# Optimization experiments

Hardware: AMD Instinct MI355X
Metric: run time of the kernel (lower is better)

Reference implementation:

```python
import jax, jax.numpy as jnp
import numpy as np

HIDDEN = 2048
HEADS = 16
HEAD_DIM = HIDDEN // HEADS  # 128
SCALE = 1.0 / float(np.sqrt(HEAD_DIM))
B, S = 2, 2048


def setup_inputs() -> dict:
    key = jax.random.key(0)
    ks = jax.random.split(key, 5)
    return {
        "x": jax.random.normal(ks[0], (B, S, HIDDEN), dtype=jnp.float32),
        "q_w": jax.random.normal(ks[1], (HIDDEN, HIDDEN), dtype=jnp.float32) * (HIDDEN ** -0.5),
        "k_w": jax.random.normal(ks[2], (HEAD_DIM, HIDDEN), dtype=jnp.float32) * (HIDDEN ** -0.5),
        "v_w": jax.random.normal(ks[3], (HEAD_DIM, HIDDEN), dtype=jnp.float32) * (HIDDEN ** -0.5),
        "o_w": jax.random.normal(ks[4], (HIDDEN, HIDDEN), dtype=jnp.float32) * (HIDDEN ** -0.5),
    }


def reference(x, q_w, k_w, v_w, o_w):
    b, s, _ = x.shape
    # torch F.linear: x @ W^T with W [out, in]
    q = (x @ q_w.T).reshape(b, s, HEADS, HEAD_DIM).transpose(0, 2, 1, 3)  # [B,H,S,D]
    k = x @ k_w.T  # [B,S,D] single shared KV head
    v = x @ v_w.T  # [B,S,D]
    # scores: [B,H,S,S] -- explicit O(S^2) materialization as in the source
    scores = jnp.einsum('bhqd,bkd->bhqk', q, k) * SCALE
    # softmax in float32 then cast back (matches dtype=torch.float32 then type_as)
    attn = jax.nn.softmax(scores.astype(jnp.float32), axis=-1).astype(q.dtype)
    out = jnp.einsum('bhqk,bkd->bhqd', attn, v)  # [B,H,S,D]
    out = out.transpose(0, 2, 1, 3).reshape(b, s, HIDDEN)
    return out @ o_w.T
```

## Files before the change

### kernel.cpp

```cpp
#include <hip/hip_runtime.h>
#include <stdint.h>

#define HID 2048
#define DHEAD 128
#define SEQL 2048
#define C2 0.1275187981510609f
#define MOFF 8.0f

typedef __attribute__((ext_vector_type(4))) float f32x4;
typedef __attribute__((ext_vector_type(8))) short s16x8;

__device__ __forceinline__ unsigned short bf16_rne(float f) {
  union { float f; unsigned u; } v; v.f = f;
  return (unsigned short)((v.u + 0x7FFFu + ((v.u >> 16) & 1u)) >> 16);
}

__device__ __forceinline__ void gload_lds16(const void* g, void* l) {
  __builtin_amdgcn_global_load_lds(
      (__attribute__((address_space(1))) unsigned int*)(void*)g,
      (__attribute__((address_space(3))) unsigned int*)l, 16, 0, 0);
}

__device__ __forceinline__ void cvt8(const float* __restrict__ in,
                                     unsigned short* __restrict__ out, int k) {
  const f32x4* p = (const f32x4*)in;
  f32x4 a = p[2 * k], b = p[2 * k + 1];
  union { s16x8 v; unsigned short s[8]; } o;
  o.s[0] = bf16_rne(a[0]); o.s[1] = bf16_rne(a[1]);
  o.s[2] = bf16_rne(a[2]); o.s[3] = bf16_rne(a[3]);
  o.s[4] = bf16_rne(b[0]); o.s[5] = bf16_rne(b[1]);
  o.s[6] = bf16_rne(b[2]); o.s[7] = bf16_rne(b[3]);
  ((s16x8*)out)[k] = o.v;
}

__global__ __launch_bounds__(256) void cvt_bf16_k(const float* __restrict__ in,
                                                  unsigned short* __restrict__ out,
                                                  int n8) {
  int i = blockIdx.x * 256 + threadIdx.x;
  if (i >= n8) return;
  cvt8(in, out, i);
}

__global__ __launch_bounds__(256) void cvt4_k(
    const float* __restrict__ s0, unsigned short* __restrict__ d0, int n0,
    const float* __restrict__ s1, unsigned short* __restrict__ d1, int n1,
    const float* __restrict__ s2, unsigned short* __restrict__ d2, int n2,
    const float* __restrict__ s3, unsigned short* __restrict__ d3, int n3) {
  int i = blockIdx.x * 256 + threadIdx.x;
  if (i < n0) { cvt8(s0, d0, i); return; }
  i -= n0;
  if (i < n1) { cvt8(s1, d1, i); return; }
  i -= n1;
  if (i < n2) { cvt8(s2, d2, i); return; }
  i -= n2;
  if (i < n3) { cvt8(s3, d3, i); return; }
}

template <int LOG2SLOTS>
__device__ __forceinline__ void stage_tile(const unsigned short* __restrict__ src,
                                           int ld, char* smem, int t) {
  int w = t >> 6;
#pragma unroll
  for (int i = 0; i < 4; ++i) {
    int c = i * 256 + t;
    int row = c >> LOG2SLOTS;
    int slot = c & ((1 << LOG2SLOTS) - 1);
    gload_lds16(src + row * ld + ((slot ^ (row & 7)) << 3),
                smem + (i * 256 + w * 64) * 16);
  }
}

template <int MODE>
__global__ __launch_bounds__(256, 2) void gemm_bt(
    const unsigned short* __restrict__ A, const unsigned short* __restrict__ Bw,
    void* __restrict__ Cout, int M, int N, int K,
    unsigned short* __restrict__ Kb, unsigned short* __restrict__ Vt) {
  __shared__ char As[2][16384];
  __shared__ char Bs[2][16384];
  int t = threadIdx.x;
  int lane = t & 63, w = t >> 6;
  int wm = w >> 1, wn = w & 1;
  int l15 = lane & 15, l4 = lane >> 4;

  int gdx = gridDim.x;
  int nwg = gdx * gridDim.y;
  int bid = blockIdx.y * gdx + blockIdx.x;
  int q8 = nwg >> 3;
  int swz = (bid & 7) * q8 + (bid >> 3);
  int tm = (swz / gdx) * 128, tn = (swz % gdx) * 128;

  f32x4 acc[4][4] = {};

  stage_tile<3>(A + tm * K, K, As[0], t);
  stage_tile<3>(Bw + tn * K, K, Bs[0], t);
  asm volatile("s_waitcnt vmcnt(0)" ::: "memory");
  __builtin_amdgcn_s_barrier();

  int nk = K >> 6;
  for (int ki = 0; ki < nk; ++ki) {
    int cur = ki & 1;
    if (ki + 1 < nk) {
      stage_tile<3>(A + tm * K + (ki + 1) * 64, K, As[cur ^ 1], t);
      stage_tile<3>(Bw + tn * K + (ki + 1) * 64, K, Bs[cur ^ 1], t);
    }
    const char* as = As[cur];
    const char* bs = Bs[cur];
    s16x8 af[4][2], bfr[4][2];
#pragma unroll
    for (int m = 0; m < 4; ++m)
#pragma unroll
      for (int kk = 0; kk < 2; ++kk) {
        int row = wm * 64 + m * 16 + l15;
        af[m][kk] = *(const s16x8*)(as + row * 128 + (((kk * 4 + l4) ^ (row & 7)) << 4));
      }
#pragma unroll
    for (int n = 0; n < 4; ++n)
#pragma unroll
      for (int kk = 0; kk < 2; ++kk) {
        int row = wn * 64 + n * 16 + l15;
        bfr[n][kk] = *(const s16x8*)(bs + row * 128 + (((kk * 4 + l4) ^ (row & 7)) << 4));
      }
    __builtin_amdgcn_s_setprio(1);
#pragma unroll
    for (int m = 0; m < 4; ++m)
#pragma unroll
      for (int n = 0; n < 4; ++n)
#pragma unroll
        for (int kk = 0; kk < 2; ++kk)
          acc[m][n] = __builtin_amdgcn_mfma_f32_16x16x32_bf16(af[m][kk], bfr[n][kk],
                                                              acc[m][n], 0, 0, 0);
    __builtin_amdgcn_s_setprio(0);
    asm volatile("s_waitcnt vmcnt(0) lgkmcnt(0)" ::: "memory");
    __builtin_amdgcn_sched_barrier(0);
    __builtin_amdgcn_s_barrier();
  }

#pragma unroll
  for (int m = 0; m < 4; ++m)
#pragma unroll
    for (int n = 0; n < 4; ++n) {
      int col = tn + wn * 64 + n * 16 + l15;
#pragma unroll
      for (int j = 0; j < 4; ++j) {
        int row = tm + wm * 64 + m * 16 + l4 * 4 + j;
        float v = acc[m][n][j];
        if (MODE == 1) {
          ((float*)Cout)[row * N + col] = v;
        } else {
          if (col < 2048) {
            ((unsigned short*)Cout)[row * 2048 + col] = bf16_rne(v);
          } else if (col < 2176) {
            Kb[row * 128 + (col - 2048)] = bf16_rne(v);
          } else {
            int d = col - 2176, bb = row >> 11, s = row & 2047;
            Vt[((bb * 128 + d) << 11) + s] = bf16_rne(v);
          }
        }
      }
    }
}

__global__ __launch_bounds__(256, 2) void attn_k(
    const unsigned short* __restrict__ Q, const unsigned short* __restrict__ Kb,
    const unsigned short* __restrict__ Vt, unsigned short* __restrict__ AO) {
  __shared__ char Ks[2][16384];
  __shared__ char Vs[2][16384];
  int t = threadIdx.x;
  int lane = t & 63, w = t >> 6;
  int l15 = lane & 15, l4 = lane >> 4;
  int qt = blockIdx.x, bh = blockIdx.y;
  int b = bh >> 4, h = bh & 15;
  int qg = b * SEQL + qt * 128 + w * 32;

  s16x8 qf[2][4];
#pragma unroll
  for (int m = 0; m < 2; ++m)
#pragma unroll
    for (int kc = 0; kc < 4; ++kc)
      qf[m][kc] = *(const s16x8*)(Q + (qg + m * 16 + l15) * HID + h * DHEAD + kc * 32 + l4 * 8);

  union { s16x8 v; unsigned short s[8]; } one_;
#pragma unroll
  for (int i = 0; i < 8; ++i) one_.s[i] = 0x3F80;
  const s16x8 ones = one_.v;

  f32x4 oacc[2][9] = {};

  {
#pragma unroll
    for (int i = 0; i < 4; ++i) {
      int c = i * 256 + t, row = c >> 4, slot = c & 15;
      gload_lds16(Kb + (b * SEQL + row) * DHEAD + ((slot ^ (row & 7)) << 3),
                  Ks[0] + (i * 256 + w * 64) * 16);
    }
#pragma unroll
    for (int i = 0; i < 4; ++i) {
      int c = i * 256 + t, row = c >> 3, slot = c & 7;
      gload_lds16(Vt + (b * DHEAD + row) * SEQL + ((slot ^ (row & 7)) << 3),
                  Vs[0] + (i * 256 + w * 64) * 16);
    }
  }
  asm volatile("s_waitcnt vmcnt(0)" ::: "memory");
  __builtin_amdgcn_s_barrier();

  for (int kv = 0; kv < SEQL; kv += 64) {
    int cur = (kv >> 6) & 1;
    if (kv + 64 < SEQL) {
#pragma unroll
      for (int i = 0; i < 4; ++i) {
        int c = i * 256 + t, row = c >> 4, slot = c & 15;
        gload_lds16(Kb + (b * SEQL + kv + 64 + row) * DHEAD + ((slot ^ (row & 7)) << 3),
                    Ks[cur ^ 1] + (i * 256 + w * 64) * 16);
      }
#pragma unroll
      for (int i = 0; i < 4; ++i) {
        int c = i * 256 + t, row = c >> 3, slot = c & 7;
        gload_lds16(Vt + (b * DHEAD + row) * SEQL + kv + 64 + ((slot ^ (row & 7)) << 3),
                    Vs[cur ^ 1] + (i * 256 + w * 64) * 16);
      }
    }

    const char* ks = Ks[cur];
    const char* vs = Vs[cur];
    char* Psw = Ks[cur] + w * 4096;

    f32x4 sacc[2][4] = {};
    __builtin_amdgcn_s_setprio(1);
#pragma unroll
    for (int n = 0; n < 4; ++n) {
      int krow = n * 16 + l15;
#pragma unroll
      for (int kc = 0; kc < 4; ++kc) {
        s16x8 kf = *(const s16x8*)(ks + krow * 256 + (((kc * 4 + l4) ^ (krow & 7)) << 4));
        sacc[0][n] = __builtin_amdgcn_mfma_f32_16x16x32_bf16(qf[0][kc], kf, sacc[0][n], 0, 0, 0);
        sacc[1][n] = __builtin_amdgcn_mfma_f32_16x16x32_bf16(qf[1][kc], kf, sacc[1][n], 0, 0, 0);
      }
    }
    __builtin_amdgcn_s_setprio(0);

    asm volatile("s_waitcnt lgkmcnt(0)" ::: "memory");
    __builtin_amdgcn_sched_barrier(0);
    __builtin_amdgcn_s_barrier();

#pragma unroll
    for (int m = 0; m < 2; ++m)
#pragma unroll
      for (int n = 0; n < 4; ++n) {
        int pcol = n * 16 + l15;
#pragma unroll
        for (int j = 0; j < 4; ++j) {
          float p = __builtin_amdgcn_exp2f(__builtin_fmaf(sacc[m][n][j], C2, -MOFF));
          int prow = m * 16 + l4 * 4 + j;
          *(unsigned short*)(Psw + prow * 128 + (((pcol >> 3) ^ (prow & 7)) << 4) +
                             (pcol & 7) * 2) = bf16_rne(p);
        }
      }

    asm volatile("s_waitcnt lgkmcnt(0)" ::: "memory");
    __builtin_amdgcn_sched_barrier(0);

#pragma unroll
    for (int kc2 = 0; kc2 < 2; ++kc2) {
      s16x8 pa[2];
#pragma unroll
      for (int m = 0; m < 2; ++m) {
        int row = m * 16 + l15;
        pa[m] = *(const s16x8*)(Psw + row * 128 + (((kc2 * 4 + l4) ^ (row & 7)) << 4));
      }
      __builtin_amdgcn_s_setprio(1);
#pragma unroll
      for (int n = 0; n < 8; ++n) {
        int vrow = n * 16 + l15;
        s16x8 vf = *(const s16x8*)(vs + vrow * 128 + (((kc2 * 4 + l4) ^ (vrow & 7)) << 4));
        oacc[0][n] = __builtin_amdgcn_mfma_f32_16x16x32_bf16(pa[0], vf, oacc[0][n], 0, 0, 0);
        oacc[1][n] = __builtin_amdgcn_mfma_f32_16x16x32_bf16(pa[1], vf, oacc[1][n], 0, 0, 0);
      }
      oacc[0][8] = __builtin_amdgcn_mfma_f32_16x16x32_bf16(pa[0], ones, oacc[0][8], 0, 0, 0);
      oacc[1][8] = __builtin_amdgcn_mfma_f32_16x16x32_bf16(pa[1], ones, oacc[1][8], 0, 0, 0);
      __builtin_amdgcn_s_setprio(0);
    }

    asm volatile("s_waitcnt vmcnt(0) lgkmcnt(0)" ::: "memory");
    __builtin_amdgcn_sched_barrier(0);
    __builtin_amdgcn_s_barrier();
  }

#pragma unroll
  for (int m = 0; m < 2; ++m) {
    float inv[4];
#pragma unroll
    for (int j = 0; j < 4; ++j) inv[j] = 1.f / oacc[m][8][j];
#pragma unroll
    for (int n = 0; n < 8; ++n) {
      int col = h * DHEAD + n * 16 + l15;
#pragma unroll
      for (int j = 0; j < 4; ++j) {
        int row = qg + m * 16 + l4 * 4 + j;
        AO[row * HID + col] = bf16_rne(oacc[m][n][j] * inv[j]);
      }
    }
  }
}

extern "C" void kernel_launch(void* const* d_in, const int* in_sizes, int n_in,
                              void* d_out, int out_size, void* d_ws, size_t ws_size,
                              hipStream_t stream) {
  const float* x  = (const float*)d_in[0];
  const float* qw = (const float*)d_in[1];
  const float* kw = (const float*)d_in[2];
  const float* vw = (const float*)d_in[3];
  const float* ow = (const float*)d_in[4];

  char* ws = (char*)d_ws;
  unsigned short* xb   = (unsigned short*)(ws);
  unsigned short* qwb  = (unsigned short*)(ws + 16777216);
  unsigned short* owb  = qwb;
  unsigned short* kvwb = (unsigned short*)(ws + 25165824);
  unsigned short* Qb   = (unsigned short*)(ws + 26214400);
  unsigned short* Kbuf = (unsigned short*)(ws + 42991616);
  unsigned short* Vtb  = (unsigned short*)(ws + 44040192);
  unsigned short* AOb  = xb;

  cvt4_k<<<6400, 256, 0, stream>>>(x, xb, 1048576, qw, qwb, 524288,
                                   kw, kvwb, 32768, vw, kvwb + 262144, 32768);

  gemm_bt<0><<<dim3(18, 32), 256, 0, stream>>>(xb, qwb, Qb, 4096, 2304, 2048, Kbuf, Vtb);
  cvt_bf16_k<<<2048, 256, 0, stream>>>(ow, owb, 524288);
  attn_k<<<dim3(16, 32), 256, 0, stream>>>(Qb, Kbuf, Vtb, AOb);
  gemm_bt<1><<<dim3(16, 32), 256, 0, stream>>>(AOb, owb, d_out, 4096, 2048, 2048,
                                               nullptr, nullptr);
}
```

Measured before the change: 215.6 us.

## Deepen GEMM prefetch pipeline and give attention P its own LDS buffer

```diff
diff --git a/kernel.cpp b/kernel.cpp
--- a/kernel.cpp
+++ b/kernel.cpp
@@ -9,6 +9,7 @@
 
 typedef __attribute__((ext_vector_type(4))) float f32x4;
 typedef __attribute__((ext_vector_type(8))) short s16x8;
+typedef __attribute__((ext_vector_type(2))) unsigned int u32x2;
 
 __device__ __forceinline__ unsigned short bf16_rne(float f) {
   union { float f; unsigned u; } v; v.f = f;
@@ -93,16 +94,17 @@
 
   stage_tile<3>(A + tm * K, K, As[0], t);
   stage_tile<3>(Bw + tn * K, K, Bs[0], t);
-  asm volatile("s_waitcnt vmcnt(0)" ::: "memory");
-  __builtin_amdgcn_s_barrier();
+  stage_tile<3>(A + tm * K + 64, K, As[1], t);
+  stage_tile<3>(Bw + tn * K + 64, K, Bs[1], t);
 
   int nk = K >> 6;
   for (int ki = 0; ki < nk; ++ki) {
     int cur = ki & 1;
-    if (ki + 1 < nk) {
-      stage_tile<3>(A + tm * K + (ki + 1) * 64, K, As[cur ^ 1], t);
-      stage_tile<3>(Bw + tn * K + (ki + 1) * 64, K, Bs[cur ^ 1], t);
-    }
+    if (ki < nk - 1) asm volatile("s_waitcnt vmcnt(8)" ::: "memory");
+    else             asm volatile("s_waitcnt vmcnt(0)" ::: "memory");
+    __builtin_amdgcn_sched_barrier(0);
+    __builtin_amdgcn_s_barrier();
+
     const char* as = As[cur];
     const char* bs = Bs[cur];
     s16x8 af[4][2], bfr[4][2];
@@ -120,6 +122,13 @@
         int row = wn * 64 + n * 16 + l15;
         bfr[n][kk] = *(const s16x8*)(bs + row * 128 + (((kk * 4 + l4) ^ (row & 7)) << 4));
       }
+    asm volatile("s_waitcnt lgkmcnt(0)" ::: "memory");
+    __builtin_amdgcn_sched_barrier(0);
+    __builtin_amdgcn_s_barrier();
+    if (ki + 2 < nk) {
+      stage_tile<3>(A + tm * K + (ki + 2) * 64, K, As[cur], t);
+      stage_tile<3>(Bw + tn * K + (ki + 2) * 64, K, Bs[cur], t);
+    }
     __builtin_amdgcn_s_setprio(1);
 #pragma unroll
     for (int m = 0; m < 4; ++m)
@@ -130,9 +139,6 @@
           acc[m][n] = __builtin_amdgcn_mfma_f32_16x16x32_bf16(af[m][kk], bfr[n][kk],
                                                               acc[m][n], 0, 0, 0);
     __builtin_amdgcn_s_setprio(0);
-    asm volatile("s_waitcnt vmcnt(0) lgkmcnt(0)" ::: "memory");
-    __builtin_amdgcn_sched_barrier(0);
-    __builtin_amdgcn_s_barrier();
   }
 
 #pragma unroll
@@ -165,12 +171,14 @@
     const unsigned short* __restrict__ Vt, unsigned short* __restrict__ AO) {
   __shared__ char Ks[2][16384];
   __shared__ char Vs[2][16384];
+  __shared__ char Ps[4][4096];
   int t = threadIdx.x;
   int lane = t & 63, w = t >> 6;
   int l15 = lane & 15, l4 = lane >> 4;
   int qt = blockIdx.x, bh = blockIdx.y;
   int b = bh >> 4, h = bh & 15;
   int qg = b * SEQL + qt * 128 + w * 32;
+  char* Psw = Ps[w];
 
   s16x8 qf[2][4];
 #pragma unroll
@@ -186,19 +194,17 @@
 
   f32x4 oacc[2][9] = {};
 
-  {
-#pragma unroll
-    for (int i = 0; i < 4; ++i) {
-      int c = i * 256 + t, row = c >> 4, slot = c & 15;
-      gload_lds16(Kb + (b * SEQL + row) * DHEAD + ((slot ^ (row & 7)) << 3),
-                  Ks[0] + (i * 256 + w * 64) * 16);
-    }
-#pragma unroll
-    for (int i = 0; i < 4; ++i) {
-      int c = i * 256 + t, row = c >> 3, slot = c & 7;
-      gload_lds16(Vt + (b * DHEAD + row) * SEQL + ((slot ^ (row & 7)) << 3),
-                  Vs[0] + (i * 256 + w * 64) * 16);
-    }
+#pragma unroll
+  for (int i = 0; i < 4; ++i) {
+    int c = i * 256 + t, row = c >> 4, slot = c & 15;
+    gload_lds16(Kb + (b * SEQL + row) * DHEAD + ((slot ^ (row & 7)) << 3),
+                Ks[0] + (i * 256 + w * 64) * 16);
+  }
+#pragma unroll
+  for (int i = 0; i < 4; ++i) {
+    int c = i * 256 + t, row = c >> 3, slot = c & 7;
+    gload_lds16(Vt + (b * DHEAD + row) * SEQL + ((slot ^ (row & 7)) << 3),
+                Vs[0] + (i * 256 + w * 64) * 16);
   }
   asm volatile("s_waitcnt vmcnt(0)" ::: "memory");
   __builtin_amdgcn_s_barrier();
@@ -222,9 +228,8 @@
 
     const char* ks = Ks[cur];
     const char* vs = Vs[cur];
-    char* Psw = Ks[cur] + w * 4096;
-
-    f32x4 sacc[2][4] = {};
+
+    f32x4 sacc[4][2] = {};
     __builtin_amdgcn_s_setprio(1);
 #pragma unroll
     for (int n = 0; n < 4; ++n) {
@@ -232,29 +237,30 @@
 #pragma unroll
       for (int kc = 0; kc < 4; ++kc) {
         s16x8 kf = *(const s16x8*)(ks + krow * 256 + (((kc * 4 + l4) ^ (krow & 7)) << 4));
-        sacc[0][n] = __builtin_amdgcn_mfma_f32_16x16x32_bf16(qf[0][kc], kf, sacc[0][n], 0, 0, 0);
-        sacc[1][n] = __builtin_amdgcn_mfma_f32_16x16x32_bf16(qf[1][kc], kf, sacc[1][n], 0, 0, 0);
+        sacc[n][0] = __builtin_amdgcn_mfma_f32_16x16x32_bf16(kf, qf[0][kc], sacc[n][0], 0, 0, 0);
+        sacc[n][1] = __builtin_amdgcn_mfma_f32_16x16x32_bf16(kf, qf[1][kc], sacc[n][1], 0, 0, 0);
       }
     }
     __builtin_amdgcn_s_setprio(0);
 
-    asm volatile("s_waitcnt lgkmcnt(0)" ::: "memory");
-    __builtin_amdgcn_sched_barrier(0);
-    __builtin_amdgcn_s_barrier();
-
-#pragma unroll
-    for (int m = 0; m < 2; ++m)
+#pragma unroll
+    for (int m = 0; m < 2; ++m) {
+      int q = m * 16 + l15;
+      char* rowp = Psw + q * 128;
+      int qx = q & 7;
 #pragma unroll
       for (int n = 0; n < 4; ++n) {
-        int pcol = n * 16 + l15;
-#pragma unroll
-        for (int j = 0; j < 4; ++j) {
-          float p = __builtin_amdgcn_exp2f(__builtin_fmaf(sacc[m][n][j], C2, -MOFF));
-          int prow = m * 16 + l4 * 4 + j;
-          *(unsigned short*)(Psw + prow * 128 + (((pcol >> 3) ^ (prow & 7)) << 4) +
-                             (pcol & 7) * 2) = bf16_rne(p);
-        }
-      }
+        float p0 = __builtin_amdgcn_exp2f(__builtin_fmaf(sacc[n][m][0], C2, -MOFF));
+        float p1 = __builtin_amdgcn_exp2f(__builtin_fmaf(sacc[n][m][1], C2, -MOFF));
+        float p2 = __builtin_amdgcn_exp2f(__builtin_fmaf(sacc[n][m][2], C2, -MOFF));
+        float p3 = __builtin_amdgcn_exp2f(__builtin_fmaf(sacc[n][m][3], C2, -MOFF));
+        u32x2 pk;
+        pk[0] = (unsigned)bf16_rne(p0) | ((unsigned)bf16_rne(p1) << 16);
+        pk[1] = (unsigned)bf16_rne(p2) | ((unsigned)bf16_rne(p3) << 16);
+        int off = (((2 * n + (l4 >> 1)) ^ qx) << 4) + ((l4 & 1) << 3);
+        *(u32x2*)(rowp + off) = pk;
+      }
+    }
 
     asm volatile("s_waitcnt lgkmcnt(0)" ::: "memory");
     __builtin_amdgcn_sched_barrier(0);
```

Result: faster. 198.0 us (-8.2%).
